# Kernel optimization log

Measured on AMD Instinct MI355X. Metric: run time of the kernel, lower is better.

Reference implementation:

```python
import jax, jax.numpy as jnp
import numpy as np


def setup_inputs() -> dict:
    key = jax.random.key(0)
    k1, k2 = jax.random.split(key)
    z = jax.random.normal(k1, (16, 256, 32, 32), dtype=jnp.float32)      # [B, C, H, W]
    weight = jax.random.normal(k2, (8192, 256), dtype=jnp.float32)       # [num_tokens, codebook_dim]
    return {"z": z, "weight": weight}


def reference(z, weight):
    B, C, H, W = z.shape
    # b c h w -> b h w c
    z_bhwc = jnp.transpose(z, (0, 2, 3, 1))
    z_flat = z_bhwc.reshape(-1, C)                                        # [B*H*W, C]
    # squared-euclidean distances: ||z||^2 + ||w||^2 - 2 z.w
    d = (jnp.sum(z_flat * z_flat, axis=1, keepdims=True)
         + jnp.sum(weight * weight, axis=1)
         - 2.0 * jnp.einsum('bd,nd->bn', z_flat, weight))                 # [B*H*W, N]
    encoding_indices = jnp.argmin(d, axis=1)                              # [B*H*W]
    z_q = jax.lax.stop_gradient(weight[encoding_indices])                 # detached gather
    z_out = z_bhwc.reshape(B, H * W, C)
    z_q = z_q.reshape(B, H * W, C)
    encoding_indices = encoding_indices.reshape(B, H, W)
    return (z_out, z_q, encoding_indices)
```

## Files before the change

### kernel.cpp

```cpp
#include <hip/hip_runtime.h>
#include <hip/hip_bf16.h>
#include <cstddef>
#include <cstdint>

typedef unsigned short u16;

#define Mtok  16384
#define Ncode 8192
#define Kdim  256
#define NSPLIT 8
#define NPER  (Ncode / NSPLIT)
#define NT    (NPER / 128)
#define TH_MARGIN 1.0f
#define RCHUNK 256
#define RNCH  (Ncode / RCHUNK)

typedef __bf16 bf16x8 __attribute__((ext_vector_type(8)));
typedef float  f32x4  __attribute__((ext_vector_type(4)));

#define LDSP(p) ((__attribute__((address_space(3))) void*)(p))
#define GPTR(p) ((const __attribute__((address_space(1))) void*)(p))

__device__ __forceinline__ u16 f2bf(float x) {
    __hip_bfloat16 h = __float2bfloat16(x);
    return *reinterpret_cast<u16*>(&h);
}

__global__ __launch_bounds__(256) void k_prep(const float* __restrict__ z,
        float* __restrict__ z_out, u16* __restrict__ sh, int* __restrict__ count) {
    __shared__ float tile[32][33];
    const int b  = blockIdx.z;
    const int c0 = blockIdx.y * 32;
    const int p0 = blockIdx.x * 32;
    const int tx = threadIdx.x;
    const int ty = threadIdx.y;
    if (b == 0 && c0 == 0 && p0 == 0 && tx == 0 && ty == 0) count[0] = 0;
    const float* src = z + ((size_t)b * Kdim + c0) * 1024 + p0;
#pragma unroll
    for (int i = 0; i < 32; i += 8)
        tile[ty + i][tx] = src[(size_t)(ty + i) * 1024 + tx];
    __syncthreads();
#pragma unroll
    for (int i = 0; i < 32; i += 8) {
        const float v = tile[tx][ty + i];
        const size_t m = (size_t)b * 1024 + p0 + ty + i;
        const int    c = c0 + tx;
        z_out[m * Kdim + c] = v;
        sh[m * Kdim + c] = f2bf(-2.0f * v);
    }
}

__global__ __launch_bounds__(64) void k_wsplit(const float* __restrict__ w,
        float* __restrict__ wnorm, u16* __restrict__ wh) {
    const int row  = blockIdx.x;
    const int lane = threadIdx.x;
    const float4 v = ((const float4*)(w + (size_t)row * Kdim))[lane];
    float s = v.x * v.x + v.y * v.y + v.z * v.z + v.w * v.w;
#pragma unroll
    for (int off = 32; off > 0; off >>= 1)
        s += __shfl_down(s, off, 64);
    if (lane == 0) wnorm[row] = s;
    ushort4 ph;
    u16* hp = (u16*)&ph;
    hp[0] = f2bf(v.x); hp[1] = f2bf(v.y); hp[2] = f2bf(v.z); hp[3] = f2bf(v.w);
    *(ushort4*)(wh + (size_t)row * Kdim + lane * 4) = ph;
}

__global__ __launch_bounds__(256, 2) void k_mfma(
        const u16* __restrict__ sh, const u16* __restrict__ wh,
        const float* __restrict__ wnorm,
        float* __restrict__ pv1, int* __restrict__ pi1,
        float* __restrict__ pv2, int* __restrict__ pi2,
        float* __restrict__ pv3) {
    __shared__ __align__(16) u16 Bh[2][128 * 32];
    __shared__ __align__(16) float wn_lds[NPER];
    const int tid  = threadIdx.x;
    const int w    = tid >> 6;
    const int lane = tid & 63;
    const int l15  = lane & 15;
    const int q    = lane >> 4;
    const int y    = blockIdx.x & 7;
    const int x    = blockIdx.x >> 3;
    const int m0   = x * 128;
    const int n0   = y * NPER;
    const int srow = lane >> 2;
    const int sq   = lane & 3;
    const int sqg  = sq ^ ((srow >> 1) & 3);
    const int qsw  = (q ^ ((l15 >> 1) & 3)) * 8;

    bf16x8 ah[8][2];
#pragma unroll
    for (int ks = 0; ks < 8; ++ks)
#pragma unroll
        for (int i = 0; i < 2; ++i) {
            const size_t ra = (size_t)(m0 + w * 32 + i * 16 + l15) * Kdim
                              + ks * 32 + q * 8;
            ah[ks][i] = *(const bf16x8*)(sh + ra);
        }
    __builtin_amdgcn_global_load_lds(GPTR(wnorm + n0 + w * 256 + lane * 4),
                                     LDSP(wn_lds + w * 256), 16, 0, 0);
#pragma unroll
    for (int rr = 0; rr < 2; ++rr) {
        const int kk = rr * 32;
#pragma unroll
        for (int t = 0; t < 2; ++t) {
            const int r  = w * 32 + t * 16 + srow;
            const int lb = (w * 32 + t * 16) * 32;
            const size_t gb = (size_t)(n0 + r) * Kdim + kk + sqg * 8;
            __builtin_amdgcn_global_load_lds(GPTR(wh + gb), LDSP(&Bh[rr][lb]), 16, 0, 0);
        }
    }

    float v1[8], v2[8], v3[8]; int i1[8], i2[8];
#pragma unroll
    for (int s = 0; s < 8; ++s) {
        v1[s] = 3.0e38f; v2[s] = 3.0e38f; v3[s] = 3.0e38f;
        i1[s] = 0x7fffffff; i2[s] = 0x7fffffff;
    }

    f32x4 acc[2][8];
#pragma unroll 1
    for (int nt = 0; nt < NT; ++nt) {
        const int nb = n0 + nt * 128;
#pragma unroll
        for (int ks = 0; ks < 8; ++ks) {
            const int rr  = nt * 8 + ks;
            const int par = rr & 1;
            if (rr == NT * 8 - 1) {
                asm volatile("s_waitcnt vmcnt(0)" ::: "memory");
            } else {
                asm volatile("s_waitcnt vmcnt(2)" ::: "memory");
            }
            __builtin_amdgcn_s_barrier();
            if (ks == 0) {
#pragma unroll
                for (int j = 0; j < 8; ++j) {
                    const float wv = wn_lds[nt * 128 + j * 16 + l15];
#pragma unroll
                    for (int i = 0; i < 2; ++i) {
                        acc[i][j][0] = wv; acc[i][j][1] = wv;
                        acc[i][j][2] = wv; acc[i][j][3] = wv;
                    }
                }
            }
            __builtin_amdgcn_s_setprio(1);
#pragma unroll
            for (int j = 0; j < 8; ++j) {
                const bf16x8 bh_ = *(const bf16x8*)&Bh[par][(j * 16 + l15) * 32 + qsw];
                acc[0][j] = __builtin_amdgcn_mfma_f32_16x16x32_bf16(ah[ks][0], bh_, acc[0][j], 0, 0, 0);
                acc[1][j] = __builtin_amdgcn_mfma_f32_16x16x32_bf16(ah[ks][1], bh_, acc[1][j], 0, 0, 0);
            }
            __builtin_amdgcn_s_setprio(0);
            asm volatile("s_waitcnt lgkmcnt(0)" ::: "memory");
            __builtin_amdgcn_s_barrier();
            if (rr + 2 < NT * 8) {
                const int rr2 = rr + 2;
                const int nb2 = n0 + (rr2 >> 3) * 128;
                const int kk2 = (rr2 & 7) * 32;
#pragma unroll
                for (int t = 0; t < 2; ++t) {
                    const int r  = w * 32 + t * 16 + srow;
                    const int lb = (w * 32 + t * 16) * 32;
                    const size_t gb = (size_t)(nb2 + r) * Kdim + kk2 + sqg * 8;
                    __builtin_amdgcn_global_load_lds(GPTR(wh + gb), LDSP(&Bh[par][lb]), 16, 0, 0);
                }
            }
        }
#pragma unroll
        for (int i = 0; i < 2; ++i)
#pragma unroll
            for (int r = 0; r < 4; ++r) {
                const int s = i * 4 + r;
#pragma unroll
                for (int j = 0; j < 8; ++j) {
                    const float d   = acc[i][j][r];
                    const int   idx = nb + j * 16 + l15;
                    const bool  b1  = d < v1[s];
                    const bool  b2  = d < v2[s];
                    v3[s] = b2 ? v2[s] : fminf(v3[s], d);
                    v2[s] = b1 ? v1[s] : (b2 ? d : v2[s]);
                    i2[s] = b1 ? i1[s] : (b2 ? idx : i2[s]);
                    v1[s] = b1 ? d : v1[s];
                    i1[s] = b1 ? idx : i1[s];
                }
            }
    }
#pragma unroll
    for (int msk = 1; msk < 16; msk <<= 1) {
#pragma unroll
        for (int s = 0; s < 8; ++s) {
            const float b1v = __shfl_xor(v1[s], msk, 64);
            const int   b1i = __shfl_xor(i1[s], msk, 64);
            const float b2v = __shfl_xor(v2[s], msk, 64);
            const int   b2i = __shfl_xor(i2[s], msk, 64);
            const float b3v = __shfl_xor(v3[s], msk, 64);
            const bool keepA = (v1[s] < b1v) || (v1[s] == b1v && i1[s] < b1i);
            const float w1 = keepA ? v1[s] : b1v;  const int wi1 = keepA ? i1[s] : b1i;
            const float l1 = keepA ? b1v : v1[s];  const int li1 = keepA ? b1i : i1[s];
            const float c2 = keepA ? v2[s] : b2v;  const int ci2 = keepA ? i2[s] : b2i;
            const bool t2 = (l1 < c2) || (l1 == c2 && li1 < ci2);
            const float w2 = t2 ? l1 : c2;         const int wi2 = t2 ? li1 : ci2;
            const float w3 = fminf(fminf(fmaxf(v2[s], b1v), fmaxf(v1[s], b2v)),
                                   fminf(v3[s], b3v));
            v1[s] = w1; i1[s] = wi1; v2[s] = w2; i2[s] = wi2; v3[s] = w3;
        }
    }
    if (l15 == 0) {
#pragma unroll
        for (int i = 0; i < 2; ++i)
#pragma unroll
            for (int r = 0; r < 4; ++r) {
                const int s = i * 4 + r;
                const int m = m0 + w * 32 + i * 16 + q * 4 + r;
                pv1[(size_t)y * Mtok + m] = v1[s];
                pi1[(size_t)y * Mtok + m] = i1[s];
                pv2[(size_t)y * Mtok + m] = v2[s];
                pi2[(size_t)y * Mtok + m] = i2[s];
                pv3[(size_t)y * Mtok + m] = v3[s];
            }
    }
}

__global__ __launch_bounds__(256) void k_merge(
        const float* __restrict__ pv1, const int* __restrict__ pi1,
        const float* __restrict__ pv2, const int* __restrict__ pi2,
        const float* __restrict__ pv3, int* __restrict__ fidx,
        int* __restrict__ flag, int* __restrict__ cands,
        int* __restrict__ list, int* __restrict__ count) {
    const int t = blockIdx.x * 256 + threadIdx.x;
    float a1[NSPLIT], a2[NSPLIT], a3[NSPLIT];
    int   x1[NSPLIT], x2[NSPLIT];
#pragma unroll
    for (int s = 0; s < NSPLIT; ++s) {
        a1[s] = pv1[(size_t)s * Mtok + t];
        x1[s] = pi1[(size_t)s * Mtok + t];
        a2[s] = pv2[(size_t)s * Mtok + t];
        x2[s] = pi2[(size_t)s * Mtok + t];
        a3[s] = pv3[(size_t)s * Mtok + t];
    }
    float gb1 = 3.0e38f; int gi1 = 0x7fffffff;
#pragma unroll
    for (int s = 0; s < NSPLIT; ++s) {
        const bool wn = (a1[s] < gb1) || (a1[s] == gb1 && x1[s] < gi1);
        gb1 = wn ? a1[s] : gb1;
        gi1 = wn ? x1[s] : gi1;
    }
    const float lim = gb1 + TH_MARGIN;
    bool full = false;
#pragma unroll
    for (int s = 0; s < NSPLIT; ++s) full |= (a3[s] < lim);
    int nc = 0;
#pragma unroll
    for (int s = 0; s < NSPLIT; ++s) {
        if (a1[s] < lim) cands[(size_t)t * 16 + nc++] = x1[s];
        if (a2[s] < lim) cands[(size_t)t * 16 + nc++] = x2[s];
    }
    fidx[t] = gi1;
    int f = 0;
    if (full) {
        f = -1;
        const int p = atomicAdd(count, 1);
        list[p] = t;
    } else if (nc >= 2) {
        f = nc;
    }
    flag[t] = f;
}

__global__ __launch_bounds__(256) void k_rescue(
        const float* __restrict__ z_out, const float* __restrict__ w,
        const float* __restrict__ wnorm, const int* __restrict__ list,
        const int* __restrict__ count,
        float* __restrict__ pcv, int* __restrict__ pci) {
    const int bx   = blockIdx.x;
    const int tid  = threadIdx.x;
    const int wv   = tid >> 6;
    const int lane = tid & 63;
    __shared__ float rv[4];
    __shared__ int   ri[4];
    const int cnt = count[0];
    for (int it = blockIdx.y; it < cnt; it += gridDim.y) {
        const int t = list[it];
        const float4 zv = *(const float4*)(z_out + (size_t)t * Kdim + lane * 4);
        float bd = 3.0e38f; int bn = 0x7fffffff;
#pragma unroll 4
        for (int i = 0; i < RCHUNK / 4; ++i) {
            const int n = bx * RCHUNK + i * 4 + wv;
            const float4 wr = *(const float4*)(w + (size_t)n * Kdim + lane * 4);
            float s = fmaf(wr.x, zv.x, fmaf(wr.y, zv.y,
                      fmaf(wr.z, zv.z, wr.w * zv.w)));
#pragma unroll
            for (int msk = 1; msk < 64; msk <<= 1)
                s += __shfl_xor(s, msk, 64);
            const float d = wnorm[n] - 2.0f * s;
            if (d < bd) { bd = d; bn = n; }
        }
        if (lane == 0) { rv[wv] = bd; ri[wv] = bn; }
        __syncthreads();
        if (tid == 0) {
            float b = rv[0]; int bi = ri[0];
#pragma unroll
            for (int k = 1; k < 4; ++k)
                if (rv[k] < b || (rv[k] == b && ri[k] < bi)) { b = rv[k]; bi = ri[k]; }
            pcv[(size_t)t * RNCH + bx] = b;
            pci[(size_t)t * RNCH + bx] = bi;
        }
        __syncthreads();
    }
}

__global__ __launch_bounds__(256) void k_gather(
        const float* __restrict__ z_out, const float* __restrict__ w,
        const float* __restrict__ wnorm, const int* __restrict__ fidx,
        const int* __restrict__ flag, const int* __restrict__ cands,
        const float* __restrict__ pcv, const int* __restrict__ pci,
        float* __restrict__ zq, float* __restrict__ idx_out) {
    const int token = blockIdx.x * 4 + (threadIdx.x >> 6);
    const int lane  = threadIdx.x & 63;
    const int f = flag[token];
    int bi = fidx[token];
    if (f == -1) {
        float v = 3.0e38f; int ii = 0x7fffffff;
        if (lane < RNCH) {
            v  = pcv[(size_t)token * RNCH + lane];
            ii = pci[(size_t)token * RNCH + lane];
        }
#pragma unroll
        for (int msk = 1; msk < 64; msk <<= 1) {
            const float ov = __shfl_xor(v, msk, 64);
            const int   oi = __shfl_xor(ii, msk, 64);
            if (ov < v || (ov == v && oi < ii)) { v = ov; ii = oi; }
        }
        bi = ii;
    } else if (f > 0) {
        const float4 zv = *(const float4*)(z_out + (size_t)token * Kdim + lane * 4);
        float bv = 3.0e38f; int bn = 0x7fffffff;
#pragma unroll 1
        for (int c = 0; c < f; ++c) {
            const int n = cands[(size_t)token * 16 + c];
            const float4 wr = *(const float4*)(w + (size_t)n * Kdim + lane * 4);
            float s = fmaf(wr.x, zv.x, fmaf(wr.y, zv.y,
                      fmaf(wr.z, zv.z, wr.w * zv.w)));
#pragma unroll
            for (int msk = 1; msk < 64; msk <<= 1)
                s += __shfl_xor(s, msk, 64);
            const float d = wnorm[n] - 2.0f * s;
            if (d < bv || (d == bv && n < bn)) { bv = d; bn = n; }
        }
        bi = bn;
    }
    const float4 u = *(const float4*)(w + (size_t)bi * Kdim + lane * 4);
    *(float4*)(zq + (size_t)token * Kdim + lane * 4) = u;
    if (lane == 0) idx_out[token] = (float)bi;
}

extern "C" void kernel_launch(void* const* d_in, const int* in_sizes, int n_in,
                              void* d_out, int out_size, void* d_ws, size_t ws_size,
                              hipStream_t stream) {
    const float* z = (const float*)d_in[0];
    const float* w = (const float*)d_in[1];

    float* z_out  = (float*)d_out;
    float* zq     = z_out + (size_t)Mtok * Kdim;
    float* idxout = zq + (size_t)Mtok * Kdim;

    char* ws = (char*)d_ws;
    u16*   sh    = (u16*)ws;                       ws += (size_t)Mtok * Kdim * 2;
    u16*   wh    = (u16*)ws;                       ws += (size_t)Ncode * Kdim * 2;
    float* wnorm = (float*)ws;                     ws += (size_t)Ncode * 4;
    float* pv1   = (float*)ws;                     ws += (size_t)NSPLIT * Mtok * 4;
    int*   pi1   = (int*)ws;                       ws += (size_t)NSPLIT * Mtok * 4;
    float* pv2   = (float*)ws;                     ws += (size_t)NSPLIT * Mtok * 4;
    int*   pi2   = (int*)ws;                       ws += (size_t)NSPLIT * Mtok * 4;
    float* pv3   = (float*)ws;                     ws += (size_t)NSPLIT * Mtok * 4;
    int*   fidx  = (int*)ws;                       ws += (size_t)Mtok * 4;
    int*   flag  = (int*)ws;                       ws += (size_t)Mtok * 4;
    int*   cands = (int*)ws;                       ws += (size_t)Mtok * 16 * 4;
    int*   list  = (int*)ws;                       ws += (size_t)Mtok * 4;
    int*   count = (int*)ws;                       ws += 256;
    float* pcv   = (float*)ws;                     ws += (size_t)Mtok * RNCH * 4;
    int*   pci   = (int*)ws;                       ws += (size_t)Mtok * RNCH * 4;

    k_prep<<<dim3(1024 / 32, Kdim / 32, 16), dim3(32, 8), 0, stream>>>(z, z_out, sh, count);
    k_wsplit<<<dim3(Ncode), dim3(64), 0, stream>>>(w, wnorm, wh);
    k_mfma<<<dim3(128 * NSPLIT), dim3(256), 0, stream>>>(sh, wh, wnorm,
                                                         pv1, pi1, pv2, pi2, pv3);
    k_merge<<<dim3(Mtok / 256), dim3(256), 0, stream>>>(pv1, pi1, pv2, pi2, pv3,
                                                        fidx, flag, cands, list, count);
    k_rescue<<<dim3(RNCH, 64), dim3(256), 0, stream>>>(z_out, w, wnorm, list, count,
                                                       pcv, pci);
    k_gather<<<dim3(Mtok / 4), dim3(256), 0, stream>>>(z_out, w, wnorm, fidx, flag,
                                                       cands, pcv, pci, zq, idxout);
}
```

Baseline: 224.7 us.

## Widen B-tile K stage to 64 and track top-2 instead of top-3

Doubles the per-stage LDS tile of codebook rows from 32 to 64 K-elements with a new XOR swizzle, halving the number of barrier/wait stages in the MFMA loop. It also reduces per-split tracking from best-3 to best-2 values (one index), cutting registers, shuffles and partial-output traffic in the MFMA and merge kernels. The trade-off is that any split whose second-best falls within the margin now sends the token to the full rescue path instead of adding a second candidate, which may increase rescue work.

```diff
diff --git a/kernel.cpp b/kernel.cpp
--- a/kernel.cpp
+++ b/kernel.cpp
@@ -69,10 +69,8 @@
 __global__ __launch_bounds__(256, 2) void k_mfma(
         const u16* __restrict__ sh, const u16* __restrict__ wh,
         const float* __restrict__ wnorm,
-        float* __restrict__ pv1, int* __restrict__ pi1,
-        float* __restrict__ pv2, int* __restrict__ pi2,
-        float* __restrict__ pv3) {
-    __shared__ __align__(16) u16 Bh[2][128 * 32];
+        float* __restrict__ pv1, int* __restrict__ pi1, float* __restrict__ pv2) {
+    __shared__ __align__(16) u16 Bh[2][128 * 64];
     __shared__ __align__(16) float wn_lds[NPER];
     const int tid  = threadIdx.x;
     const int w    = tid >> 6;
@@ -83,10 +81,9 @@
     const int x    = blockIdx.x >> 3;
     const int m0   = x * 128;
     const int n0   = y * NPER;
-    const int srow = lane >> 2;
-    const int sq   = lane & 3;
-    const int sqg  = sq ^ ((srow >> 1) & 3);
-    const int qsw  = (q ^ ((l15 >> 1) & 3)) * 8;
+    const int srow8 = lane >> 3;
+    const int sqg8  = (lane & 7) ^ srow8;
+    const int rsw   = l15 & 7;
 
     bf16x8 ah[8][2];
 #pragma unroll
@@ -101,38 +98,35 @@
                                      LDSP(wn_lds + w * 256), 16, 0, 0);
 #pragma unroll
     for (int rr = 0; rr < 2; ++rr) {
-        const int kk = rr * 32;
-#pragma unroll
-        for (int t = 0; t < 2; ++t) {
-            const int r  = w * 32 + t * 16 + srow;
-            const int lb = (w * 32 + t * 16) * 32;
-            const size_t gb = (size_t)(n0 + r) * Kdim + kk + sqg * 8;
-            __builtin_amdgcn_global_load_lds(GPTR(wh + gb), LDSP(&Bh[rr][lb]), 16, 0, 0);
-        }
-    }
-
-    float v1[8], v2[8], v3[8]; int i1[8], i2[8];
-#pragma unroll
-    for (int s = 0; s < 8; ++s) {
-        v1[s] = 3.0e38f; v2[s] = 3.0e38f; v3[s] = 3.0e38f;
-        i1[s] = 0x7fffffff; i2[s] = 0x7fffffff;
-    }
+        const int kk = rr * 64;
+#pragma unroll
+        for (int t = 0; t < 4; ++t) {
+            const int row = w * 32 + t * 8 + srow8;
+            const size_t gb = (size_t)(n0 + row) * Kdim + kk + sqg8 * 8;
+            __builtin_amdgcn_global_load_lds(GPTR(wh + gb),
+                LDSP(&Bh[rr][(w * 32 + t * 8) * 64]), 16, 0, 0);
+        }
+    }
+
+    float v1[8], v2[8]; int i1[8];
+#pragma unroll
+    for (int s = 0; s < 8; ++s) { v1[s] = 3.0e38f; v2[s] = 3.0e38f; i1[s] = 0x7fffffff; }
 
     f32x4 acc[2][8];
 #pragma unroll 1
     for (int nt = 0; nt < NT; ++nt) {
         const int nb = n0 + nt * 128;
 #pragma unroll
-        for (int ks = 0; ks < 8; ++ks) {
-            const int rr  = nt * 8 + ks;
+        for (int rq = 0; rq < 4; ++rq) {
+            const int rr  = nt * 4 + rq;
             const int par = rr & 1;
-            if (rr == NT * 8 - 1) {
+            if (rr == NT * 4 - 1) {
                 asm volatile("s_waitcnt vmcnt(0)" ::: "memory");
             } else {
-                asm volatile("s_waitcnt vmcnt(2)" ::: "memory");
+                asm volatile("s_waitcnt vmcnt(4)" ::: "memory");
             }
             __builtin_amdgcn_s_barrier();
-            if (ks == 0) {
+            if (rq == 0) {
 #pragma unroll
                 for (int j = 0; j < 8; ++j) {
                     const float wv = wn_lds[nt * 128 + j * 16 + l15];
@@ -145,24 +139,30 @@
             }
             __builtin_amdgcn_s_setprio(1);
 #pragma unroll
-            for (int j = 0; j < 8; ++j) {
-                const bf16x8 bh_ = *(const bf16x8*)&Bh[par][(j * 16 + l15) * 32 + qsw];
-                acc[0][j] = __builtin_amdgcn_mfma_f32_16x16x32_bf16(ah[ks][0], bh_, acc[0][j], 0, 0, 0);
-                acc[1][j] = __builtin_amdgcn_mfma_f32_16x16x32_bf16(ah[ks][1], bh_, acc[1][j], 0, 0, 0);
+            for (int ks2 = 0; ks2 < 2; ++ks2) {
+                const int kidx = rq * 2 + ks2;
+#pragma unroll
+                for (int j = 0; j < 8; ++j) {
+                    const int slot = (ks2 * 4 + q) ^ rsw;
+                    const bf16x8 bh_ = *(const bf16x8*)
+                        &Bh[par][(j * 16 + l15) * 64 + slot * 8];
+                    acc[0][j] = __builtin_amdgcn_mfma_f32_16x16x32_bf16(ah[kidx][0], bh_, acc[0][j], 0, 0, 0);
+                    acc[1][j] = __builtin_amdgcn_mfma_f32_16x16x32_bf16(ah[kidx][1], bh_, acc[1][j], 0, 0, 0);
+                }
             }
             __builtin_amdgcn_s_setprio(0);
             asm volatile("s_waitcnt lgkmcnt(0)" ::: "memory");
             __builtin_amdgcn_s_barrier();
-            if (rr + 2 < NT * 8) {
+            if (rr + 2 < NT * 4) {
                 const int rr2 = rr + 2;
-                const int nb2 = n0 + (rr2 >> 3) * 128;
-                const int kk2 = (rr2 & 7) * 32;
-#pragma unroll
-                for (int t = 0; t < 2; ++t) {
-                    const int r  = w * 32 + t * 16 + srow;
-                    const int lb = (w * 32 + t * 16) * 32;
-                    const size_t gb = (size_t)(nb2 + r) * Kdim + kk2 + sqg * 8;
-                    __builtin_amdgcn_global_load_lds(GPTR(wh + gb), LDSP(&Bh[par][lb]), 16, 0, 0);
+                const int nb2 = n0 + (rr2 >> 2) * 128;
+                const int kk2 = (rr2 & 3) * 64;
+#pragma unroll
+                for (int t = 0; t < 4; ++t) {
+                    const int row = w * 32 + t * 8 + srow8;
+                    const size_t gb = (size_t)(nb2 + row) * Kdim + kk2 + sqg8 * 8;
+                    __builtin_amdgcn_global_load_lds(GPTR(wh + gb),
+                        LDSP(&Bh[par][(w * 32 + t * 8) * 64]), 16, 0, 0);
                 }
             }
         }
@@ -176,10 +176,7 @@
                     const float d   = acc[i][j][r];
                     const int   idx = nb + j * 16 + l15;
                     const bool  b1  = d < v1[s];
-                    const bool  b2  = d < v2[s];
-                    v3[s] = b2 ? v2[s] : fminf(v3[s], d);
-                    v2[s] = b1 ? v1[s] : (b2 ? d : v2[s]);
-                    i2[s] = b1 ? i1[s] : (b2 ? idx : i2[s]);
+                    v2[s] = b1 ? v1[s] : fminf(v2[s], d);
                     v1[s] = b1 ? d : v1[s];
                     i1[s] = b1 ? idx : i1[s];
                 }
@@ -192,17 +189,11 @@
             const float b1v = __shfl_xor(v1[s], msk, 64);
             const int   b1i = __shfl_xor(i1[s], msk, 64);
             const float b2v = __shfl_xor(v2[s], msk, 64);
-            const int   b2i = __shfl_xor(i2[s], msk, 64);
-            const float b3v = __shfl_xor(v3[s], msk, 64);
             const bool keepA = (v1[s] < b1v) || (v1[s] == b1v && i1[s] < b1i);
-            const float w1 = keepA ? v1[s] : b1v;  const int wi1 = keepA ? i1[s] : b1i;
-            const float l1 = keepA ? b1v : v1[s];  const int li1 = keepA ? b1i : i1[s];
-            const float c2 = keepA ? v2[s] : b2v;  const int ci2 = keepA ? i2[s] : b2i;
-            const bool t2 = (l1 < c2) || (l1 == c2 && li1 < ci2);
-            const float w2 = t2 ? l1 : c2;         const int wi2 = t2 ? li1 : ci2;
-            const float w3 = fminf(fminf(fmaxf(v2[s], b1v), fmaxf(v1[s], b2v)),
-                                   fminf(v3[s], b3v));
-            v1[s] = w1; i1[s] = wi1; v2[s] = w2; i2[s] = wi2; v3[s] = w3;
+            const float lose = keepA ? b1v : v1[s];
+            v1[s] = keepA ? v1[s] : b1v;
+            i1[s] = keepA ? i1[s] : b1i;
+            v2[s] = fminf(fminf(v2[s], b2v), lose);
         }
     }
     if (l15 == 0) {
@@ -215,28 +206,23 @@
                 pv1[(size_t)y * Mtok + m] = v1[s];
                 pi1[(size_t)y * Mtok + m] = i1[s];
                 pv2[(size_t)y * Mtok + m] = v2[s];
-                pi2[(size_t)y * Mtok + m] = i2[s];
-                pv3[(size_t)y * Mtok + m] = v3[s];
             }
     }
 }
 
 __global__ __launch_bounds__(256) void k_merge(
         const float* __restrict__ pv1, const int* __restrict__ pi1,
-        const float* __restrict__ pv2, const int* __restrict__ pi2,
-        const float* __restrict__ pv3, int* __restrict__ fidx,
+        const float* __restrict__ pv2, int* __restrict__ fidx,
         int* __restrict__ flag, int* __restrict__ cands,
         int* __restrict__ list, int* __restrict__ count) {
     const int t = blockIdx.x * 256 + threadIdx.x;
-    float a1[NSPLIT], a2[NSPLIT], a3[NSPLIT];
-    int   x1[NSPLIT], x2[NSPLIT];
+    float a1[NSPLIT], a2[NSPLIT];
+    int   x1[NSPLIT];
 #pragma unroll
     for (int s = 0; s < NSPLIT; ++s) {
         a1[s] = pv1[(size_t)s * Mtok + t];
         x1[s] = pi1[(size_t)s * Mtok + t];
         a2[s] = pv2[(size_t)s * Mtok + t];
-        x2[s] = pi2[(size_t)s * Mtok + t];
-        a3[s] = pv3[(size_t)s * Mtok + t];
     }
     float gb1 = 3.0e38f; int gi1 = 0x7fffffff;
 #pragma unroll
@@ -248,13 +234,11 @@
     const float lim = gb1 + TH_MARGIN;
     bool full = false;
 #pragma unroll
-    for (int s = 0; s < NSPLIT; ++s) full |= (a3[s] < lim);
+    for (int s = 0; s < NSPLIT; ++s) full |= (a2[s] < lim);
     int nc = 0;
 #pragma unroll
-    for (int s = 0; s < NSPLIT; ++s) {
+    for (int s = 0; s < NSPLIT; ++s)
         if (a1[s] < lim) cands[(size_t)t * 16 + nc++] = x1[s];
-        if (a2[s] < lim) cands[(size_t)t * 16 + nc++] = x2[s];
-    }
     fidx[t] = gi1;
     int f = 0;
     if (full) {
@@ -371,8 +355,6 @@
     float* pv1   = (float*)ws;                     ws += (size_t)NSPLIT * Mtok * 4;
     int*   pi1   = (int*)ws;                       ws += (size_t)NSPLIT * Mtok * 4;
     float* pv2   = (float*)ws;                     ws += (size_t)NSPLIT * Mtok * 4;
-    int*   pi2   = (int*)ws;                       ws += (size_t)NSPLIT * Mtok * 4;
-    float* pv3   = (float*)ws;                     ws += (size_t)NSPLIT * Mtok * 4;
     int*   fidx  = (int*)ws;                       ws += (size_t)Mtok * 4;
     int*   flag  = (int*)ws;                       ws += (size_t)Mtok * 4;
     int*   cands = (int*)ws;                       ws += (size_t)Mtok * 16 * 4;
@@ -384,8 +366,8 @@
     k_prep<<<dim3(1024 / 32, Kdim / 32, 16), dim3(32, 8), 0, stream>>>(z, z_out, sh, count);
     k_wsplit<<<dim3(Ncode), dim3(64), 0, stream>>>(w, wnorm, wh);
     k_mfma<<<dim3(128 * NSPLIT), dim3(256), 0, stream>>>(sh, wh, wnorm,
-                                                         pv1, pi1, pv2, pi2, pv3);
-    k_merge<<<dim3(Mtok / 256), dim3(256), 0, stream>>>(pv1, pi1, pv2, pi2, pv3,
+                                                         pv1, pi1, pv2);
+    k_merge<<<dim3(Mtok / 256), dim3(256), 0, stream>>>(pv1, pi1, pv2,
                                                         fidx, flag, cands, list, count);
     k_rescue<<<dim3(RNCH, 64), dim3(256), 0, stream>>>(z_out, w, wnorm, list, count,
                                                        pcv, pci);
```

Result: slower. 326.4 us (+45.3%).
